# Optimization experiments

Measured on AMD Instinct MI355X. Metric: run time of the kernel, lower is better.

## Reference

```python
import jax, jax.numpy as jnp
import numpy as np

PS = 16          # patch size == conv kernel == stride
EPS = 1e-5       # BatchNorm eps (torch default)


def setup_inputs() -> dict:
    key = jax.random.key(0)
    ks = jax.random.split(key, 12)
    B, Cin, H = 64, 3, 256
    D, Dm = 3, 768                      # private_depth, hidden_dim
    P = (H // PS) ** 2                  # num_patches = 256

    x = jax.random.normal(ks[0], (B, Cin, H, H), jnp.float32)
    # patch-embed conv: weight [O, I, kh, kw], bias [O]
    conv0_w = jax.random.normal(ks[1], (Dm, Cin, PS, PS), jnp.float32) * 0.02
    conv0_b = jax.random.normal(ks[2], (Dm,), jnp.float32) * 0.02
    # depth x (1x1 conv + BN): stacked params
    w1 = jax.random.normal(ks[3], (D, Dm, Dm), jnp.float32) * 0.02   # [O, I]
    b1 = jax.random.normal(ks[4], (D, Dm), jnp.float32) * 0.02
    gamma = jnp.ones((D, Dm), jnp.float32)
    beta = jnp.zeros((D, Dm), jnp.float32)
    # positional embedding [1, P, Dm]
    pos_emb = jax.random.normal(ks[5], (1, P, Dm), jnp.float32)
    # mixer Linear [out, in] + bias
    mixer_w = jax.random.normal(ks[6], (Dm, Dm), jnp.float32) * 0.02
    mixer_b = jax.random.normal(ks[7], (Dm,), jnp.float32) * 0.02
    # per-sample random permutation of the P patches (replaces randperm loop)
    perm = jax.vmap(lambda k: jax.random.permutation(k, P))(
        jax.random.split(ks[8], B)).astype(jnp.int32)

    return {"x": x, "conv0_w": conv0_w, "conv0_b": conv0_b, "w1": w1,
            "b1": b1, "gamma": gamma, "beta": beta, "pos_emb": pos_emb,
            "mixer_w": mixer_w, "mixer_b": mixer_b, "perm": perm}


def reference(x, conv0_w, conv0_b, w1, b1, gamma, beta, pos_emb,
              mixer_w, mixer_b, perm):
    B, Cin, H, W = x.shape
    hp, wp = H // PS, W // PS
    Dm = conv0_w.shape[0]

    # non-overlapping patch conv == reshape + matmul
    # x -> [B, hp*wp, Cin*PS*PS] with (c, kh, kw) flattening matching conv weight
    patches = x.reshape(B, Cin, hp, PS, wp, PS).transpose(0, 2, 4, 1, 3, 5)
    patches = patches.reshape(B, hp * wp, Cin * PS * PS)
    h = jax.nn.relu(patches @ conv0_w.reshape(Dm, -1).T + conv0_b)  # [B, P, Dm]

    # private_depth x (1x1 conv -> BN (batch stats, no running stats) -> ReLU)
    for d in range(w1.shape[0]):
        h = h @ w1[d].T + b1[d]
        mu = h.mean(axis=(0, 1))                      # per-channel over (B, H*W)
        var = ((h - mu) ** 2).mean(axis=(0, 1))       # biased variance
        h = (h - mu) * jax.lax.rsqrt(var + EPS) * gamma[d] + beta[d]
        h = jax.nn.relu(h)

    # pos embedding + mixer (ReLU -> Linear)
    h = h + pos_emb
    h = jax.nn.relu(h) @ mixer_w.T + mixer_b          # [B, P, Dm]

    # per-sample pixel shuffle: shuffled[i, j] = h[i, perm[i, j]]
    out = jnp.take_along_axis(h, perm[:, :, None].astype(jnp.int32), axis=1)
    return out
```

## Files before the change

### kernel.cpp

```cpp
#include <hip/hip_runtime.h>
#include <hip/hip_bf16.h>
#include <stdint.h>

#define M_TOT 16384
#define DM 768
#define BM 128
#define BN 192
#define NKT3 12
#define QOFF (128 * DM)

typedef __attribute__((ext_vector_type(4))) float f32x4;
typedef __attribute__((ext_vector_type(8))) short short8;
typedef __attribute__((ext_vector_type(8))) unsigned short ushort8;
typedef __attribute__((ext_vector_type(4))) unsigned short ushort4v;

__device__ __forceinline__ unsigned short f2bf(float f) {
    union { float f; unsigned u; } v; v.f = f;
    unsigned r = v.u + 0x7fffu + ((v.u >> 16) & 1u);
    return (unsigned short)(r >> 16);
}
__device__ __forceinline__ float bf2f(unsigned short h) {
    union { unsigned u; float f; } v; v.u = ((unsigned)h) << 16;
    return v.f;
}

__device__ __forceinline__ void gload_lds16(const unsigned short* g, unsigned short* l) {
    __builtin_amdgcn_global_load_lds(
        (const __attribute__((address_space(1))) void*)g,
        (__attribute__((address_space(3))) void*)l, 16, 0, 0);
}

__global__ __launch_bounds__(256)
void prepim(const float* __restrict__ cw, const float* __restrict__ w1,
            const float* __restrict__ mw, const int* __restrict__ perm,
            const float* __restrict__ x,
            unsigned short* __restrict__ wA, unsigned short* __restrict__ wD,
            unsigned short* __restrict__ wM, int* __restrict__ invp,
            unsigned short* __restrict__ patches)
{
    int b = blockIdx.x;
    if (b < 12288) {
        int t = b * 256 + threadIdx.x;
        int bp = t / 192;
        int q  = t - bp * 192;
        int c   = q >> 6;
        int kh  = (q >> 2) & 15;
        int kw0 = (q & 3) << 2;
        int bb = bp >> 8, p = bp & 255;
        int ph = p >> 4, pw = p & 15;
        const float* src = x + ((((size_t)bb * 3 + c) * 256 + ph * 16 + kh) * 256 + pw * 16 + kw0);
        f32x4 v = *(const f32x4*)src;
        ushort4v o;
        o.x = f2bf(v.x); o.y = f2bf(v.y); o.z = f2bf(v.z); o.w = f2bf(v.w);
        *(ushort4v*)(patches + (size_t)bp * DM + (q << 2)) = o;
    } else if (b < 12288 + 2880) {
        int i = (b - 12288) * 256 + threadIdx.x;
        const float* src; unsigned short* dst; int off;
        if (i < 147456)              { src = cw; dst = wA; off = i; }
        else if (i < 147456+442368)  { src = w1; dst = wD; off = i - 147456; }
        else                         { src = mw; dst = wM; off = i - 589824; }
        f32x4 v = ((const f32x4*)src)[off];
        ushort4v o;
        o.x = f2bf(v.x); o.y = f2bf(v.y); o.z = f2bf(v.z); o.w = f2bf(v.w);
        ((ushort4v*)dst)[off] = o;
    } else {
        int i = (b - 12288 - 2880) * 256 + threadIdx.x;
        int bb = i >> 8;
        invp[(bb << 8) + perm[i]] = i & 255;
    }
}

#define VM0  asm volatile("s_waitcnt vmcnt(0)" ::: "memory");
#define LGKM0 asm volatile("s_waitcnt lgkmcnt(0)" ::: "memory");
#define BARR asm volatile("s_barrier" ::: "memory");

#define PH(AB, BB, MH, KS, LOADB, PRE, POST)                                     \
  {                                                                              \
    if (LOADB) {                                                                 \
      _Pragma("unroll")                                                          \
      for (int j = 0; j < 3; ++j)                                                \
        breg[j] = *(const short8*)((const char*)Bb + (size_t)(BB) * (BN*64*2) +  \
                  (wc * 48 + j * 16 + frow) * 128 + (((KS) * 64 + fq16) ^ rswz));\
    }                                                                            \
    short8 af[4];                                                                \
    _Pragma("unroll")                                                            \
    for (int i = 0; i < 4; ++i)                                                  \
      af[i] = *(const short8*)((const char*)Aa + (size_t)(AB) * (BM*64*2) +      \
              ((MH) * 64 + i * 16 + frow) * 128 +                                \
              (((KS) * 64 + fq16) ^ rswz));                                      \
    PRE;                                                                         \
    __builtin_amdgcn_s_setprio(1);                                               \
    _Pragma("unroll")                                                            \
    for (int i = 0; i < 4; ++i)                                                  \
      _Pragma("unroll")                                                          \
      for (int j = 0; j < 3; ++j)                                                \
        acc[(MH) * 4 + i][j] = __builtin_amdgcn_mfma_f32_16x16x32_bf16(          \
            af[i], breg[j], acc[(MH) * 4 + i][j], 0, 0, 0);                      \
    __builtin_amdgcn_s_setprio(0);                                               \
    POST;                                                                        \
    BARR                                                                         \
  }

template<int EPI, int BNA>
__global__ __launch_bounds__(256, 2)
void gemm8p(const unsigned short* __restrict__ A,
            const unsigned short* __restrict__ Bw,
            const float* __restrict__ bias,
            void* __restrict__ outp,
            const int* __restrict__ invp,
            float* __restrict__ bnpart,
            const float* __restrict__ ssA)
{
    __shared__ unsigned short Aa[2][BM * 64];
    __shared__ unsigned short Bb[2][BN * 64];

    const int tid  = threadIdx.x;
    const int w    = tid >> 6;
    const int lane = tid & 63;
    const int wc = w;

    int bid = blockIdx.x;
    int nb  = (bid & 7) * 64 + (bid >> 3);
    const int tileM = nb >> 2, tileN = nb & 3;
    const int m0 = tileM * BM, n0 = tileN * BN;

    const int sRow = lane >> 3;
    const int swzc = ((lane & 7) * 16) ^ ((sRow & 7) << 4);
    const unsigned short* gA0 = A  + (size_t)(m0 + w * 32 + sRow) * DM + (swzc >> 1);
    const unsigned short* gB0 = Bw + (size_t)(n0 + w * 48 + sRow) * DM + (swzc >> 1);

    auto STAGE_A = [&](int buf, int kt) {
        #pragma unroll
        for (int j = 0; j < 4; ++j)
            gload_lds16(gA0 + (size_t)j * 8 * DM + kt * 64,
                        &Aa[buf][(w * 32 + j * 8) * 64]);
    };
    auto STAGE_B = [&](int buf, int kt) {
        #pragma unroll
        for (int j = 0; j < 6; ++j)
            gload_lds16(gB0 + (size_t)j * 8 * DM + kt * 64,
                        &Bb[buf][(w * 48 + j * 8) * 64]);
    };

    const int rRow0 = w * 32 + (lane >> 3);
    const unsigned short* gAr = A + (size_t)(m0 + rRow0) * DM + (lane & 7) * 8;
    const int wrswz = (lane >> 3) << 4;
    ushort8 aldr[4];

    auto ALOAD = [&](int t) {
        #pragma unroll
        for (int j = 0; j < 4; ++j)
            aldr[j] = *(const ushort8*)(gAr + (size_t)j * 8 * DM + t * 64);
    };
    auto XFORM = [&](int t, int tb) {
        const int k0 = t * 64 + (lane & 7) * 8;
        f32x4 sa = *(const f32x4*)(ssA + k0);
        f32x4 sb = *(const f32x4*)(ssA + k0 + 4);
        f32x4 ha = *(const f32x4*)(ssA + DM + k0);
        f32x4 hb = *(const f32x4*)(ssA + DM + k0 + 4);
        #pragma unroll
        for (int j = 0; j < 4; ++j) {
            int row = rRow0 + j * 8;
            ushort8 u = aldr[j];
            ushort8 o;
            #pragma unroll
            for (int e = 0; e < 8; ++e) {
                float f = bf2f(u[e]);
                float sc = (e < 4) ? sa[e] : sb[e - 4];
                float sh = (e < 4) ? ha[e] : hb[e - 4];
                o[e] = f2bf(fmaxf(fmaf(sc, f, sh), 0.0f));
            }
            *(ushort8*)((char*)Aa + (size_t)tb * (BM*64*2) + row * 128 +
                        (((lane & 7) * 16) ^ wrswz)) = o;
        }
    };

    const int frow = lane & 15;
    const int fq16 = (lane >> 4) * 16;
    const int rswz = (lane & 7) << 4;

    f32x4 acc[8][3] = {};
    short8 breg[3];

    if (BNA == 0) {
        STAGE_A(0, 0);
        STAGE_B(0, 0);
        VM0
        BARR
    } else {
        ALOAD(0); XFORM(0, 0);
        ALOAD(1);
        STAGE_B(0, 0);
        VM0
        LGKM0
        BARR
    }

    if (BNA == 0) {
        #pragma unroll
        for (int kt = 0; kt < NKT3; ++kt) {
            const int cb = kt & 1, nbuf = cb ^ 1;
            PH(cb, cb, 0, 0, 1, { if (kt < 11) STAGE_B(nbuf, kt + 1); }, {})
            PH(cb, cb, 1, 0, 0, { if (kt < 11) STAGE_A(nbuf, kt + 1); }, {})
            PH(cb, cb, 0, 1, 1, {}, {})
            if (kt < 11) { PH(cb, cb, 1, 1, 0, {}, { VM0 }) }
            else         { PH(cb, cb, 1, 1, 0, {}, {}) }
        }
    } else {
        #pragma unroll 2
        for (int kt = 0; kt < NKT3; ++kt) {
            const int cb = kt & 1, nbuf = cb ^ 1;
            PH(cb, cb, 0, 0, 1, { if (kt < 11) STAGE_B(nbuf, kt + 1); }, {})
            PH(cb, cb, 1, 0, 0, { if (kt < 11) XFORM(kt + 1, nbuf); },
                                { if (kt < 11) LGKM0 })
            PH(cb, cb, 0, 1, 1, {}, {})
            if (kt < 11) { PH(cb, cb, 1, 1, 0, {}, { VM0
                                                     if (kt < 10) ALOAD(kt + 2); }) }
            else         { PH(cb, cb, 1, 1, 0, {}, {}) }
        }
    }

    const int crow = (lane >> 4) * 4;
    const int ccol = lane & 15;
    const int nbase = n0 + wc * 48;

    float bv[3];
    #pragma unroll
    for (int j = 0; j < 3; ++j) bv[j] = bias[nbase + j * 16 + ccol];

    if (EPI == 0) {
        unsigned short* O = (unsigned short*)outp;
        #pragma unroll
        for (int mi = 0; mi < 8; ++mi) {
            #pragma unroll
            for (int r = 0; r < 4; ++r) {
                int m = m0 + mi * 16 + crow + r;
                unsigned short* orow = O + (size_t)m * DM + nbase + ccol;
                #pragma unroll
                for (int j = 0; j < 3; ++j)
                    orow[j * 16] = f2bf(fmaxf(acc[mi][j][r] + bv[j], 0.0f));
            }
        }
    }

    if (EPI == 2) {
        float* O = (float*)outp;
        #pragma unroll
        for (int mi = 0; mi < 8; ++mi) {
            #pragma unroll
            for (int r = 0; r < 4; ++r) {
                int m = m0 + mi * 16 + crow + r;
                int mo = (m & ~255) | invp[m];
                float* orow = O + (size_t)mo * DM + nbase + ccol;
                #pragma unroll
                for (int j = 0; j < 3; ++j)
                    orow[j * 16] = acc[mi][j][r] + bv[j];
            }
        }
    }

    if (EPI == 1) {
        unsigned short* O = (unsigned short*)outp;
        #pragma unroll
        for (int mi = 0; mi < 8; ++mi) {
            #pragma unroll
            for (int r = 0; r < 4; ++r) {
                int m = m0 + mi * 16 + crow + r;
                unsigned short* orow = O + (size_t)m * DM + nbase + ccol;
                #pragma unroll
                for (int j = 0; j < 3; ++j)
                    orow[j * 16] = f2bf(acc[mi][j][r] + bv[j]);
            }
        }
        #pragma unroll
        for (int j = 0; j < 3; ++j) {
            float s = 0.f, q = 0.f;
            #pragma unroll
            for (int mi = 0; mi < 8; ++mi)
                #pragma unroll
                for (int r = 0; r < 4; ++r) {
                    float v = acc[mi][j][r] + bv[j];
                    s += v; q += v * v;
                }
            s += __shfl_xor(s, 16); s += __shfl_xor(s, 32);
            q += __shfl_xor(q, 16); q += __shfl_xor(q, 32);
            if (lane < 16) {
                int c = nbase + j * 16 + lane;
                bnpart[(size_t)c * 128 + tileM]        = s;
                bnpart[QOFF + (size_t)c * 128 + tileM] = q;
            }
        }
    }
}

__global__ void bn_stats(const float* __restrict__ part, const float* __restrict__ gamma,
                         const float* __restrict__ beta, float* __restrict__ ss)
{
    int c = blockIdx.x * 256 + threadIdx.x;
    const float* ps = part + (size_t)c * 128;
    const float* pq = part + QOFF + (size_t)c * 128;
    float s = 0.f, q = 0.f;
    #pragma unroll 8
    for (int i = 0; i < 128; ++i) { s += ps[i]; q += pq[i]; }
    float mu  = s * (1.0f / 16384.0f);
    float var = q * (1.0f / 16384.0f) - mu * mu;
    float scale = rsqrtf(var + 1e-5f) * gamma[c];
    ss[c] = scale;
    ss[DM + c] = beta[c] - mu * scale;
}

__global__ __launch_bounds__(256)
void bnpos_apply(const unsigned short* __restrict__ hin, const float* __restrict__ ss,
                 const float* __restrict__ pos, unsigned short* __restrict__ hout)
{
    __shared__ float sc[DM], sh[DM];
    const int t = threadIdx.x;
    #pragma unroll
    for (int i = 0; i < 3; ++i) {
        sc[t + i * 256] = ss[t + i * 256];
        sh[t + i * 256] = ss[DM + t + i * 256];
    }
    __syncthreads();

    int g = blockIdx.x * 256 + t;
    int row = g / 96;
    int c0 = (g - row * 96) * 8;
    const short8 v = *(const short8*)(hin + (size_t)row * DM + c0);
    short8 o;
    #pragma unroll
    for (int e = 0; e < 8; ++e) {
        float xv = bf2f((unsigned short)v[e]);
        float y = fmaxf(xv * sc[c0 + e] + sh[c0 + e], 0.0f);
        y = fmaxf(y + pos[(row & 255) * DM + c0 + e], 0.0f);
        o[e] = (short)f2bf(y);
    }
    *(short8*)(hout + (size_t)row * DM + c0) = o;
}

extern "C" void kernel_launch(void* const* d_in, const int* in_sizes, int n_in,
                              void* d_out, int out_size, void* d_ws, size_t ws_size,
                              hipStream_t stream)
{
    (void)in_sizes; (void)n_in; (void)out_size; (void)ws_size;

    const float* x       = (const float*)d_in[0];
    const float* conv0_w = (const float*)d_in[1];
    const float* conv0_b = (const float*)d_in[2];
    const float* w1      = (const float*)d_in[3];
    const float* b1      = (const float*)d_in[4];
    const float* gamma   = (const float*)d_in[5];
    const float* beta    = (const float*)d_in[6];
    const float* pos     = (const float*)d_in[7];
    const float* mixer_w = (const float*)d_in[8];
    const float* mixer_b = (const float*)d_in[9];
    const int*   perm    = (const int*)d_in[10];

    unsigned short* actA = (unsigned short*)d_ws;
    unsigned short* actB = actA + (size_t)M_TOT * DM;
    unsigned short* wA   = actB + (size_t)M_TOT * DM;
    unsigned short* wD   = wA + DM * DM;
    unsigned short* wM   = wD + 3 * DM * DM;
    float* bnpart = (float*)(wM + DM * DM);
    float* ss     = bnpart + 2 * 128 * DM;
    int*   invp   = (int*)(ss + 2 * DM);

    prepim<<<15232, 256, 0, stream>>>(conv0_w, w1, mixer_w, perm, x,
                                      wA, wD, wM, invp, actA);

    gemm8p<0, 0><<<512, 256, 0, stream>>>(actA, wA, conv0_b, actB, nullptr,
                                          nullptr, nullptr);
    gemm8p<1, 0><<<512, 256, 0, stream>>>(actB, wD + 0 * (size_t)DM * DM, b1 + 0 * DM,
                                          actA, nullptr, bnpart, nullptr);
    bn_stats<<<3, 256, 0, stream>>>(bnpart, gamma + 0 * DM, beta + 0 * DM, ss);
    gemm8p<1, 1><<<512, 256, 0, stream>>>(actA, wD + 1 * (size_t)DM * DM, b1 + 1 * DM,
                                          actB, nullptr, bnpart, ss);
    bn_stats<<<3, 256, 0, stream>>>(bnpart, gamma + 1 * DM, beta + 1 * DM, ss);
    gemm8p<1, 1><<<512, 256, 0, stream>>>(actB, wD + 2 * (size_t)DM * DM, b1 + 2 * DM,
                                          actA, nullptr, bnpart, ss);
    bn_stats<<<3, 256, 0, stream>>>(bnpart, gamma + 2 * DM, beta + 2 * DM, ss);
    bnpos_apply<<<6144, 256, 0, stream>>>(actA, ss, pos, actB);
    gemm8p<2, 0><<<512, 256, 0, stream>>>(actB, wM, mixer_b, d_out, invp,
                                          nullptr, nullptr);
}
```

Before: 198.1 us.

## Fuse im2col patch extraction and BN+pos apply into GEMM A-loaders

The separate im2col/bf16-cast pass over the input image is removed, and the first GEMM now reads fp32 pixels directly from x in its register-staged A path and converts them to bf16 into LDS. The standalone BN-apply plus positional-embedding kernel is also removed, and that transform is folded into the mixer GEMM's A transform (XF==2). Together these drop two full activation round trips through global memory and two launches. In exchange, the first and last GEMMs now use the slower register-staged A path, and the first GEMM makes strided fp32 reads instead of direct-to-LDS bf16 loads.

```diff
diff --git a/kernel.cpp b/kernel.cpp
--- a/kernel.cpp
+++ b/kernel.cpp
@@ -31,30 +31,14 @@
 }
 
 __global__ __launch_bounds__(256)
-void prepim(const float* __restrict__ cw, const float* __restrict__ w1,
-            const float* __restrict__ mw, const int* __restrict__ perm,
-            const float* __restrict__ x,
-            unsigned short* __restrict__ wA, unsigned short* __restrict__ wD,
-            unsigned short* __restrict__ wM, int* __restrict__ invp,
-            unsigned short* __restrict__ patches)
+void prepw(const float* __restrict__ cw, const float* __restrict__ w1,
+           const float* __restrict__ mw, const int* __restrict__ perm,
+           unsigned short* __restrict__ wA, unsigned short* __restrict__ wD,
+           unsigned short* __restrict__ wM, int* __restrict__ invp)
 {
     int b = blockIdx.x;
-    if (b < 12288) {
-        int t = b * 256 + threadIdx.x;
-        int bp = t / 192;
-        int q  = t - bp * 192;
-        int c   = q >> 6;
-        int kh  = (q >> 2) & 15;
-        int kw0 = (q & 3) << 2;
-        int bb = bp >> 8, p = bp & 255;
-        int ph = p >> 4, pw = p & 15;
-        const float* src = x + ((((size_t)bb * 3 + c) * 256 + ph * 16 + kh) * 256 + pw * 16 + kw0);
-        f32x4 v = *(const f32x4*)src;
-        ushort4v o;
-        o.x = f2bf(v.x); o.y = f2bf(v.y); o.z = f2bf(v.z); o.w = f2bf(v.w);
-        *(ushort4v*)(patches + (size_t)bp * DM + (q << 2)) = o;
-    } else if (b < 12288 + 2880) {
-        int i = (b - 12288) * 256 + threadIdx.x;
+    if (b < 2880) {
+        int i = b * 256 + threadIdx.x;
         const float* src; unsigned short* dst; int off;
         if (i < 147456)              { src = cw; dst = wA; off = i; }
         else if (i < 147456+442368)  { src = w1; dst = wD; off = i - 147456; }
@@ -64,7 +48,7 @@
         o.x = f2bf(v.x); o.y = f2bf(v.y); o.z = f2bf(v.z); o.w = f2bf(v.w);
         ((ushort4v*)dst)[off] = o;
     } else {
-        int i = (b - 12288 - 2880) * 256 + threadIdx.x;
+        int i = (b - 2880) * 256 + threadIdx.x;
         int bb = i >> 8;
         invp[(bb << 8) + perm[i]] = i & 255;
     }
@@ -101,18 +85,22 @@
     BARR                                                                         \
   }
 
-template<int EPI, int BNA>
+template<int EPI, int XF>
 __global__ __launch_bounds__(256, 2)
-void gemm8p(const unsigned short* __restrict__ A,
+void gemm8p(const void* __restrict__ Asrc,
             const unsigned short* __restrict__ Bw,
             const float* __restrict__ bias,
             void* __restrict__ outp,
             const int* __restrict__ invp,
             float* __restrict__ bnpart,
-            const float* __restrict__ ssA)
+            const float* __restrict__ ssA,
+            const float* __restrict__ pos)
 {
     __shared__ unsigned short Aa[2][BM * 64];
     __shared__ unsigned short Bb[2][BN * 64];
+
+    const unsigned short* A = (const unsigned short*)Asrc;
+    const float* X = (const float*)Asrc;
 
     const int tid  = threadIdx.x;
     const int w    = tid >> 6;
@@ -146,32 +134,73 @@
     const unsigned short* gAr = A + (size_t)(m0 + rRow0) * DM + (lane & 7) * 8;
     const int wrswz = (lane >> 3) << 4;
     ushort8 aldr[4];
+    f32x4   aldf[4][2];
 
     auto ALOAD = [&](int t) {
-        #pragma unroll
-        for (int j = 0; j < 4; ++j)
-            aldr[j] = *(const ushort8*)(gAr + (size_t)j * 8 * DM + t * 64);
+        if (XF == 3) {
+            const int c  = t >> 2;
+            const int r  = (t & 3) * 64 + (lane & 7) * 8;
+            const int kh = r >> 4;
+            const int kw0 = r & 15;
+            #pragma unroll
+            for (int j = 0; j < 4; ++j) {
+                int m = m0 + rRow0 + j * 8;
+                int b = m >> 8, p = m & 255;
+                const float* src = X + ((((size_t)b * 3 + c) * 256 + (p >> 4) * 16 + kh) * 256
+                                        + (p & 15) * 16 + kw0);
+                aldf[j][0] = *(const f32x4*)src;
+                aldf[j][1] = *(const f32x4*)(src + 4);
+            }
+        } else {
+            #pragma unroll
+            for (int j = 0; j < 4; ++j)
+                aldr[j] = *(const ushort8*)(gAr + (size_t)j * 8 * DM + t * 64);
+        }
     };
     auto XFORM = [&](int t, int tb) {
-        const int k0 = t * 64 + (lane & 7) * 8;
-        f32x4 sa = *(const f32x4*)(ssA + k0);
-        f32x4 sb = *(const f32x4*)(ssA + k0 + 4);
-        f32x4 ha = *(const f32x4*)(ssA + DM + k0);
-        f32x4 hb = *(const f32x4*)(ssA + DM + k0 + 4);
-        #pragma unroll
-        for (int j = 0; j < 4; ++j) {
-            int row = rRow0 + j * 8;
-            ushort8 u = aldr[j];
-            ushort8 o;
-            #pragma unroll
-            for (int e = 0; e < 8; ++e) {
-                float f = bf2f(u[e]);
-                float sc = (e < 4) ? sa[e] : sb[e - 4];
-                float sh = (e < 4) ? ha[e] : hb[e - 4];
-                o[e] = f2bf(fmaxf(fmaf(sc, f, sh), 0.0f));
-            }
-            *(ushort8*)((char*)Aa + (size_t)tb * (BM*64*2) + row * 128 +
-                        (((lane & 7) * 16) ^ wrswz)) = o;
+        if (XF == 3) {
+            #pragma unroll
+            for (int j = 0; j < 4; ++j) {
+                int row = rRow0 + j * 8;
+                ushort8 o;
+                #pragma unroll
+                for (int e = 0; e < 8; ++e)
+                    o[e] = f2bf((e < 4) ? aldf[j][0][e] : aldf[j][1][e - 4]);
+                *(ushort8*)((char*)Aa + (size_t)tb * (BM*64*2) + row * 128 +
+                            (((lane & 7) * 16) ^ wrswz)) = o;
+            }
+        } else {
+            const int k0 = t * 64 + (lane & 7) * 8;
+            f32x4 sa = *(const f32x4*)(ssA + k0);
+            f32x4 sb = *(const f32x4*)(ssA + k0 + 4);
+            f32x4 ha = *(const f32x4*)(ssA + DM + k0);
+            f32x4 hb = *(const f32x4*)(ssA + DM + k0 + 4);
+            #pragma unroll
+            for (int j = 0; j < 4; ++j) {
+                int row = rRow0 + j * 8;
+                f32x4 pa, pb;
+                if (XF == 2) {
+                    int prow = (m0 & 255) + row;
+                    pa = *(const f32x4*)(pos + (size_t)prow * DM + k0);
+                    pb = *(const f32x4*)(pos + (size_t)prow * DM + k0 + 4);
+                }
+                ushort8 u = aldr[j];
+                ushort8 o;
+                #pragma unroll
+                for (int e = 0; e < 8; ++e) {
+                    float f = bf2f(u[e]);
+                    float sc = (e < 4) ? sa[e] : sb[e - 4];
+                    float sh = (e < 4) ? ha[e] : hb[e - 4];
+                    float y = fmaxf(fmaf(sc, f, sh), 0.0f);
+                    if (XF == 2) {
+                        float pv = (e < 4) ? pa[e] : pb[e - 4];
+                        y = fmaxf(y + pv, 0.0f);
+                    }
+                    o[e] = f2bf(y);
+                }
+                *(ushort8*)((char*)Aa + (size_t)tb * (BM*64*2) + row * 128 +
+                            (((lane & 7) * 16) ^ wrswz)) = o;
+            }
         }
     };
 
@@ -182,7 +211,7 @@
     f32x4 acc[8][3] = {};
     short8 breg[3];
 
-    if (BNA == 0) {
+    if (XF == 0) {
         STAGE_A(0, 0);
         STAGE_B(0, 0);
         VM0
@@ -196,7 +225,7 @@
         BARR
     }
 
-    if (BNA == 0) {
+    if (XF == 0) {
         #pragma unroll
         for (int kt = 0; kt < NKT3; ++kt) {
             const int cb = kt & 1, nbuf = cb ^ 1;
@@ -309,34 +338,6 @@
     ss[DM + c] = beta[c] - mu * scale;
 }
 
-__global__ __launch_bounds__(256)
-void bnpos_apply(const unsigned short* __restrict__ hin, const float* __restrict__ ss,
-                 const float* __restrict__ pos, unsigned short* __restrict__ hout)
-{
-    __shared__ float sc[DM], sh[DM];
-    const int t = threadIdx.x;
-    #pragma unroll
-    for (int i = 0; i < 3; ++i) {
-        sc[t + i * 256] = ss[t + i * 256];
-        sh[t + i * 256] = ss[DM + t + i * 256];
-    }
-    __syncthreads();
-
-    int g = blockIdx.x * 256 + t;
-    int row = g / 96;
-    int c0 = (g - row * 96) * 8;
-    const short8 v = *(const short8*)(hin + (size_t)row * DM + c0);
-    short8 o;
-    #pragma unroll
-    for (int e = 0; e < 8; ++e) {
-        float xv = bf2f((unsigned short)v[e]);
-        float y = fmaxf(xv * sc[c0 + e] + sh[c0 + e], 0.0f);
-        y = fmaxf(y + pos[(row & 255) * DM + c0 + e], 0.0f);
-        o[e] = (short)f2bf(y);
-    }
-    *(short8*)(hout + (size_t)row * DM + c0) = o;
-}
-
 extern "C" void kernel_launch(void* const* d_in, const int* in_sizes, int n_in,
                               void* d_out, int out_size, void* d_ws, size_t ws_size,
                               hipStream_t stream)
@@ -364,21 +365,19 @@
     float* ss     = bnpart + 2 * 128 * DM;
     int*   invp   = (int*)(ss + 2 * DM);
 
-    prepim<<<15232, 256, 0, stream>>>(conv0_w, w1, mixer_w, perm, x,
-                                      wA, wD, wM, invp, actA);
-
-    gemm8p<0, 0><<<512, 256, 0, stream>>>(actA, wA, conv0_b, actB, nullptr,
-                                          nullptr, nullptr);
+    prepw<<<2944, 256, 0, stream>>>(conv0_w, w1, mixer_w, perm, wA, wD, wM, invp);
+
+    gemm8p<0, 3><<<512, 256, 0, stream>>>(x, wA, conv0_b, actB, nullptr,
+                                          nullptr, nullptr, nullptr);
     gemm8p<1, 0><<<512, 256, 0, stream>>>(actB, wD + 0 * (size_t)DM * DM, b1 + 0 * DM,
-                                          actA, nullptr, bnpart, nullptr);
+                                          actA, nullptr, bnpart, nullptr, nullptr);
     bn_stats<<<3, 256, 0, stream>>>(bnpart, gamma + 0 * DM, beta + 0 * DM, ss);
     gemm8p<1, 1><<<512, 256, 0, stream>>>(actA, wD + 1 * (size_t)DM * DM, b1 + 1 * DM,
-                                          actB, nullptr, bnpart, ss);
+                                          actB, nullptr, bnpart, ss, nullptr);
     bn_stats<<<3, 256, 0, stream>>>(bnpart, gamma + 1 * DM, beta + 1 * DM, ss);
     gemm8p<1, 1><<<512, 256, 0, stream>>>(actB, wD + 2 * (size_t)DM * DM, b1 + 2 * DM,
-                                          actA, nullptr, bnpart, ss);
+                                          actA, nullptr, bnpart, ss, nullptr);
     bn_stats<<<3, 256, 0, stream>>>(bnpart, gamma + 2 * DM, beta + 2 * DM, ss);
-    bnpos_apply<<<6144, 256, 0, stream>>>(actA, ss, pos, actB);
-    gemm8p<2, 0><<<512, 256, 0, stream>>>(actB, wM, mixer_b, d_out, invp,
-                                          nullptr, nullptr);
-}
+    gemm8p<2, 2><<<512, 256, 0, stream>>>(actA, wM, mixer_b, d_out, invp,
+                                          nullptr, ss, pos);
+}
```

Result: faster. 193.6 us (-2.3%).

## Fuse patch extraction and bf16 conversion into first GEMM's A-tile loader

Applied to the files above, without the earlier changes.

The first GEMM now reads fp32 pixels straight from x, gathers patch rows and converts them to bf16 while staging into LDS. This removes the separate im2col pass that wrote a bf16 patch matrix and the GEMM's reread of it. The register-staged A loader is also restructured into double-buffered register sets, with loads issued two k-tiles ahead, and this applies to the BN-transform GEMMs as well. The cost is more registers and strided 32-byte global reads of fp32 data inside the GEMM, which could lower occupancy or hurt coalescing.

```diff
diff --git a/kernel.cpp b/kernel.cpp
--- a/kernel.cpp
+++ b/kernel.cpp
@@ -31,30 +31,14 @@
 }
 
 __global__ __launch_bounds__(256)
-void prepim(const float* __restrict__ cw, const float* __restrict__ w1,
-            const float* __restrict__ mw, const int* __restrict__ perm,
-            const float* __restrict__ x,
-            unsigned short* __restrict__ wA, unsigned short* __restrict__ wD,
-            unsigned short* __restrict__ wM, int* __restrict__ invp,
-            unsigned short* __restrict__ patches)
+void prepw(const float* __restrict__ cw, const float* __restrict__ w1,
+           const float* __restrict__ mw, const int* __restrict__ perm,
+           unsigned short* __restrict__ wA, unsigned short* __restrict__ wD,
+           unsigned short* __restrict__ wM, int* __restrict__ invp)
 {
     int b = blockIdx.x;
-    if (b < 12288) {
-        int t = b * 256 + threadIdx.x;
-        int bp = t / 192;
-        int q  = t - bp * 192;
-        int c   = q >> 6;
-        int kh  = (q >> 2) & 15;
-        int kw0 = (q & 3) << 2;
-        int bb = bp >> 8, p = bp & 255;
-        int ph = p >> 4, pw = p & 15;
-        const float* src = x + ((((size_t)bb * 3 + c) * 256 + ph * 16 + kh) * 256 + pw * 16 + kw0);
-        f32x4 v = *(const f32x4*)src;
-        ushort4v o;
-        o.x = f2bf(v.x); o.y = f2bf(v.y); o.z = f2bf(v.z); o.w = f2bf(v.w);
-        *(ushort4v*)(patches + (size_t)bp * DM + (q << 2)) = o;
-    } else if (b < 12288 + 2880) {
-        int i = (b - 12288) * 256 + threadIdx.x;
+    if (b < 2880) {
+        int i = b * 256 + threadIdx.x;
         const float* src; unsigned short* dst; int off;
         if (i < 147456)              { src = cw; dst = wA; off = i; }
         else if (i < 147456+442368)  { src = w1; dst = wD; off = i - 147456; }
@@ -64,7 +48,7 @@
         o.x = f2bf(v.x); o.y = f2bf(v.y); o.z = f2bf(v.z); o.w = f2bf(v.w);
         ((ushort4v*)dst)[off] = o;
     } else {
-        int i = (b - 12288 - 2880) * 256 + threadIdx.x;
+        int i = (b - 2880) * 256 + threadIdx.x;
         int bb = i >> 8;
         invp[(bb << 8) + perm[i]] = i & 255;
     }
@@ -101,9 +85,78 @@
     BARR                                                                         \
   }
 
-template<int EPI, int BNA>
+#define ALOADM(t, S)                                                             \
+  {                                                                              \
+    if (XF == 3) {                                                               \
+      const int c  = (t) >> 2;                                                   \
+      const int r  = ((t) & 3) * 64 + (lane & 7) * 8;                            \
+      const int kh = r >> 4;                                                     \
+      const int kw0 = r & 15;                                                    \
+      _Pragma("unroll")                                                          \
+      for (int j = 0; j < 4; ++j) {                                              \
+        int m = m0 + rRow0 + j * 8;                                              \
+        int b = m >> 8, p = m & 255;                                             \
+        const float* src = X + ((((size_t)b * 3 + c) * 256 + (p >> 4) * 16 + kh) \
+                                * 256 + (p & 15) * 16 + kw0);                    \
+        aldf##S[j][0] = *(const f32x4*)src;                                      \
+        aldf##S[j][1] = *(const f32x4*)(src + 4);                                \
+      }                                                                          \
+    } else {                                                                     \
+      _Pragma("unroll")                                                          \
+      for (int j = 0; j < 4; ++j)                                                \
+        aldr##S[j] = *(const ushort8*)(gAr + (size_t)j * 8 * DM + (t) * 64);     \
+    }                                                                            \
+  }
+
+#define XFORMM(t, tb, S)                                                         \
+  {                                                                              \
+    if (XF == 3) {                                                               \
+      _Pragma("unroll")                                                          \
+      for (int j = 0; j < 4; ++j) {                                              \
+        int row = rRow0 + j * 8;                                                 \
+        ushort8 o;                                                               \
+        _Pragma("unroll")                                                        \
+        for (int e = 0; e < 8; ++e)                                              \
+          o[e] = f2bf((e < 4) ? aldf##S[j][0][e] : aldf##S[j][1][e - 4]);        \
+        *(ushort8*)((char*)Aa + (size_t)(tb) * (BM*64*2) + row * 128 +           \
+                    (((lane & 7) * 16) ^ wrswz)) = o;                            \
+      }                                                                          \
+    } else {                                                                     \
+      const int k0 = (t) * 64 + (lane & 7) * 8;                                  \
+      f32x4 sa = *(const f32x4*)(ssA + k0);                                      \
+      f32x4 sb = *(const f32x4*)(ssA + k0 + 4);                                  \
+      f32x4 ha = *(const f32x4*)(ssA + DM + k0);                                 \
+      f32x4 hb = *(const f32x4*)(ssA + DM + k0 + 4);                             \
+      _Pragma("unroll")                                                          \
+      for (int j = 0; j < 4; ++j) {                                              \
+        int row = rRow0 + j * 8;                                                 \
+        ushort8 u = aldr##S[j];                                                  \
+        ushort8 o;                                                               \
+        _Pragma("unroll")                                                        \
+        for (int e = 0; e < 8; ++e) {                                            \
+          float f = bf2f(u[e]);                                                  \
+          float sc = (e < 4) ? sa[e] : sb[e - 4];                                \
+          float sh = (e < 4) ? ha[e] : hb[e - 4];                                \
+          o[e] = f2bf(fmaxf(fmaf(sc, f, sh), 0.0f));                             \
+        }                                                                        \
+        *(ushort8*)((char*)Aa + (size_t)(tb) * (BM*64*2) + row * 128 +           \
+                    (((lane & 7) * 16) ^ wrswz)) = o;                            \
+      }                                                                          \
+    }                                                                            \
+  }
+
+#define XTILE(kt, CB, LS, XS)                                                    \
+    PH(CB, CB, 0, 0, 1, { if ((kt) < 11) STAGE_B((CB) ^ 1, (kt) + 1);            \
+                          if ((kt) < 10) ALOADM((kt) + 2, LS) }, {})             \
+    PH(CB, CB, 1, 0, 0, { if ((kt) < 11) XFORMM((kt) + 1, (CB) ^ 1, XS) },       \
+                        { if ((kt) < 11) LGKM0 })                                \
+    PH(CB, CB, 0, 1, 1, {}, {})                                                  \
+    if ((kt) < 11) { PH(CB, CB, 1, 1, 0, {}, { VM0 }) }                          \
+    else           { PH(CB, CB, 1, 1, 0, {}, {}) }
+
+template<int EPI, int XF>
 __global__ __launch_bounds__(256, 2)
-void gemm8p(const unsigned short* __restrict__ A,
+void gemm8p(const void* __restrict__ Asrc,
             const unsigned short* __restrict__ Bw,
             const float* __restrict__ bias,
             void* __restrict__ outp,
@@ -114,6 +167,9 @@
     __shared__ unsigned short Aa[2][BM * 64];
     __shared__ unsigned short Bb[2][BN * 64];
 
+    const unsigned short* A = (const unsigned short*)Asrc;
+    const float* X = (const float*)Asrc;
+
     const int tid  = threadIdx.x;
     const int w    = tid >> 6;
     const int lane = tid & 63;
@@ -145,35 +201,8 @@
     const int rRow0 = w * 32 + (lane >> 3);
     const unsigned short* gAr = A + (size_t)(m0 + rRow0) * DM + (lane & 7) * 8;
     const int wrswz = (lane >> 3) << 4;
-    ushort8 aldr[4];
-
-    auto ALOAD = [&](int t) {
-        #pragma unroll
-        for (int j = 0; j < 4; ++j)
-            aldr[j] = *(const ushort8*)(gAr + (size_t)j * 8 * DM + t * 64);
-    };
-    auto XFORM = [&](int t, int tb) {
-        const int k0 = t * 64 + (lane & 7) * 8;
-        f32x4 sa = *(const f32x4*)(ssA + k0);
-        f32x4 sb = *(const f32x4*)(ssA + k0 + 4);
-        f32x4 ha = *(const f32x4*)(ssA + DM + k0);
-        f32x4 hb = *(const f32x4*)(ssA + DM + k0 + 4);
-        #pragma unroll
-        for (int j = 0; j < 4; ++j) {
-            int row = rRow0 + j * 8;
-            ushort8 u = aldr[j];
-            ushort8 o;
-            #pragma unroll
-            for (int e = 0; e < 8; ++e) {
-                float f = bf2f(u[e]);
-                float sc = (e < 4) ? sa[e] : sb[e - 4];
-                float sh = (e < 4) ? ha[e] : hb[e - 4];
-                o[e] = f2bf(fmaxf(fmaf(sc, f, sh), 0.0f));
-            }
-            *(ushort8*)((char*)Aa + (size_t)tb * (BM*64*2) + row * 128 +
-                        (((lane & 7) * 16) ^ wrswz)) = o;
-        }
-    };
+    ushort8 aldr0[4], aldr1[4];
+    f32x4   aldf0[4][2], aldf1[4][2];
 
     const int frow = lane & 15;
     const int fq16 = (lane >> 4) * 16;
@@ -182,21 +211,22 @@
     f32x4 acc[8][3] = {};
     short8 breg[3];
 
-    if (BNA == 0) {
+    if (XF == 0) {
         STAGE_A(0, 0);
         STAGE_B(0, 0);
         VM0
         BARR
     } else {
-        ALOAD(0); XFORM(0, 0);
-        ALOAD(1);
+        ALOADM(0, 0)
+        ALOADM(1, 1)
         STAGE_B(0, 0);
+        XFORMM(0, 0, 0)
         VM0
         LGKM0
         BARR
     }
 
-    if (BNA == 0) {
+    if (XF == 0) {
         #pragma unroll
         for (int kt = 0; kt < NKT3; ++kt) {
             const int cb = kt & 1, nbuf = cb ^ 1;
@@ -207,16 +237,11 @@
             else         { PH(cb, cb, 1, 1, 0, {}, {}) }
         }
     } else {
-        #pragma unroll 2
-        for (int kt = 0; kt < NKT3; ++kt) {
-            const int cb = kt & 1, nbuf = cb ^ 1;
-            PH(cb, cb, 0, 0, 1, { if (kt < 11) STAGE_B(nbuf, kt + 1); }, {})
-            PH(cb, cb, 1, 0, 0, { if (kt < 11) XFORM(kt + 1, nbuf); },
-                                { if (kt < 11) LGKM0 })
-            PH(cb, cb, 0, 1, 1, {}, {})
-            if (kt < 11) { PH(cb, cb, 1, 1, 0, {}, { VM0
-                                                     if (kt < 10) ALOAD(kt + 2); }) }
-            else         { PH(cb, cb, 1, 1, 0, {}, {}) }
+        for (int kp = 0; kp < 6; ++kp) {
+            const int kte = 2 * kp;
+            XTILE(kte, 0, 0, 1)
+            const int kto = kte + 1;
+            XTILE(kto, 1, 1, 0)
         }
     }
 
@@ -364,10 +389,9 @@
     float* ss     = bnpart + 2 * 128 * DM;
     int*   invp   = (int*)(ss + 2 * DM);
 
-    prepim<<<15232, 256, 0, stream>>>(conv0_w, w1, mixer_w, perm, x,
-                                      wA, wD, wM, invp, actA);
-
-    gemm8p<0, 0><<<512, 256, 0, stream>>>(actA, wA, conv0_b, actB, nullptr,
+    prepw<<<2944, 256, 0, stream>>>(conv0_w, w1, mixer_w, perm, wA, wD, wM, invp);
+
+    gemm8p<0, 3><<<512, 256, 0, stream>>>(x, wA, conv0_b, actB, nullptr,
                                           nullptr, nullptr);
     gemm8p<1, 0><<<512, 256, 0, stream>>>(actB, wD + 0 * (size_t)DM * DM, b1 + 0 * DM,
                                           actA, nullptr, bnpart, nullptr);
```

Result: faster. 185.8 us (-6.2%).
